# Optimization experiments

Measured on AMD Instinct MI355X. Metric: run time of the kernel, lower is better.

Reference implementation:

```python
import jax, jax.numpy as jnp
import numpy as np

B, T, E, H, S = 4, 4096, 1024, 16, 64
D = E // H  # head_dim = 64
ROPE_BASE = 10000.0


def _rotate_half(x):
    # interleaved rotate: out[..., 2i] = -x[..., 2i+1]; out[..., 2i+1] = x[..., 2i]
    x1 = x[..., ::2]
    x2 = x[..., 1::2]
    return jnp.stack([-x2, x1], axis=-1).reshape(x.shape)


def _rope_cos_sin(t, d):
    inv_freq = 1.0 / (ROPE_BASE ** (jnp.arange(0, d, 2, dtype=jnp.float32) / d))
    freqs = jnp.arange(t, dtype=jnp.float32)[:, None] * inv_freq[None, :]  # [t, d/2]
    emb = jnp.concatenate([freqs, freqs], axis=-1)  # [t, d]
    # broadcast over batch and heads for q/k of shape [b, t, h, d]
    return jnp.cos(emb)[None, :, None, :], jnp.sin(emb)[None, :, None, :]


def setup_inputs() -> dict:
    key = jax.random.key(0)
    ks = jax.random.split(key, 6)
    s = E ** -0.5
    return {
        "x": jax.random.normal(ks[0], (B, T, E), dtype=jnp.float32),
        "Wq": jax.random.normal(ks[1], (E, E), dtype=jnp.float32) * s,
        "Wk": jax.random.normal(ks[2], (E, E), dtype=jnp.float32) * s,
        "Wv": jax.random.normal(ks[3], (E, E), dtype=jnp.float32) * s,
        "Wout": jax.random.normal(ks[4], (E, E), dtype=jnp.float32) * s,
        "slot_keys": jax.random.normal(ks[5], (H, S, D), dtype=jnp.float32) * (D ** -0.5),
    }


def reference(x, Wq, Wk, Wv, Wout, slot_keys):
    b, t, e = x.shape
    h, s_slots, d = slot_keys.shape
    scale = d ** -0.5

    q = (x @ Wq.T).reshape(b, t, h, d)
    k = (x @ Wk.T).reshape(b, t, h, d)
    v = (x @ Wv.T).reshape(b, t, h, d)

    cos, sin = _rope_cos_sin(t, d)
    q = q * cos + _rotate_half(q) * sin
    k = k * cos + _rotate_half(k) * sin

    # write pass: route each token's value into memory slots
    write_logits = jnp.einsum('bthd,hsd->bths', k, slot_keys) * scale
    write_weights = jax.nn.softmax(write_logits, axis=-1)  # write_temperature = 1.0
    slot_state = jnp.einsum('bths,bthd->bshd', write_weights, v) / t

    # read pass: query the slot memory
    read_logits = jnp.einsum('bthd,bshd->bths', q, slot_state) * scale
    read_weights = jax.nn.softmax(read_logits, axis=-1)  # read_temperature = 1.0
    read_out = jnp.einsum('bths,bshd->bthd', read_weights, slot_state)

    return read_out.reshape(b, t, e) @ Wout.T
```

## Files before the change

### kernel.cpp

```cpp
#include <hip/hip_runtime.h>
#include <cstdint>
#include <cstddef>

#define BB 4
#define TT 4096
#define EE 1024
#define HH 16
#define SSLOTS 64
#define DD 64
#define MM (BB*TT)

typedef unsigned short u16;
typedef __attribute__((ext_vector_type(8))) short s16x8;
typedef __attribute__((ext_vector_type(4))) float f32x4;
typedef __attribute__((ext_vector_type(8))) unsigned short us8v;
typedef __attribute__((ext_vector_type(4))) unsigned short us4v;

#define MFMA16(a, b, c) __builtin_amdgcn_mfma_f32_16x16x32_bf16((a), (b), (c), 0, 0, 0)

__device__ __forceinline__ u16 f2bf(float x) {
  union { float f; uint32_t u; } c; c.f = x;
  uint32_t u = c.u;
  u += 0x7fffu + ((u >> 16) & 1u);
  return (u16)(u >> 16);
}

__device__ __forceinline__ float bf2f(u16 x) {
  union { uint32_t u; float f; } c; c.u = ((uint32_t)x) << 16;
  return c.f;
}

__device__ __forceinline__ void async16(const void* g, void* l) {
  auto lp = reinterpret_cast<__attribute__((address_space(3))) void*>(
      reinterpret_cast<uintptr_t>(l));
  auto gp = reinterpret_cast<const __attribute__((address_space(1))) void*>(
      reinterpret_cast<uintptr_t>(g));
  __builtin_amdgcn_global_load_lds(gp, lp, 16, 0, 0);
}

__device__ __forceinline__ us8v rope8(us8v kv, const float* __restrict__ rcp,
                                      const float* __restrict__ rsp) {
  float e[8];
#pragma unroll
  for (int m = 0; m < 8; ++m) e[m] = bf2f((u16)kv[m]);
  us8v o;
#pragma unroll
  for (int j = 0; j < 4; ++j) {
    float c0 = rcp[2 * j], c1 = rcp[2 * j + 1];
    float s0 = rsp[2 * j], s1 = rsp[2 * j + 1];
    o[2 * j]     = f2bf(e[2 * j] * c0 - e[2 * j + 1] * s0);
    o[2 * j + 1] = f2bf(e[2 * j + 1] * c1 + e[2 * j] * s1);
  }
  return o;
}

__global__ __launch_bounds__(256) void k_cvt(const float* __restrict__ s,
                                             u16* __restrict__ d, int n) {
  int i = (blockIdx.x * 256 + threadIdx.x) * 4;
  if (i >= n) return;
  float4 v = *(const float4*)(s + i);
  us4v o = { f2bf(v.x), f2bf(v.y), f2bf(v.z), f2bf(v.w) };
  *(us4v*)(d + i) = o;
}

__global__ __launch_bounds__(256) void k_rope(float* __restrict__ rc, float* __restrict__ rs) {
  int i = blockIdx.x * 256 + threadIdx.x;
  if (i >= TT * 32) return;
  int t = i >> 5, f = i & 31;
  double invf = pow(10000.0, -(double)(2 * f) / 64.0);
  double th = fmod((double)t * invf, 6.28318530717958647692528676655900577);
  rc[i] = (float)cos(th);
  rs[i] = (float)sin(th);
}

__device__ __forceinline__ void gemm_tile_128(const u16* __restrict__ Ablk,
                                              const u16* __restrict__ Bblk,
                                              int K, u16* As, u16* Bs,
                                              f32x4 acc[4][4]) {
  const int tid = threadIdx.x;
  const int lane = tid & 63, wave = tid >> 6;
  const int l16 = lane & 15, q8 = (lane >> 4) * 8;
  const int wm = (wave >> 1) * 64, wn = (wave & 1) * 64;
  const int ar = tid >> 2, ac = (tid & 3) * 8;
  const u16* Ag0 = Ablk + (size_t)ar * K + ac;
  const u16* Ag1 = Ablk + (size_t)(ar + 64) * K + ac;
  const u16* Bg0 = Bblk + (size_t)ar * K + ac;
  const u16* Bg1 = Bblk + (size_t)(ar + 64) * K + ac;
  u16* Al0 = As + ar * 32 + ac;
  u16* Al1 = As + (ar + 64) * 32 + ac;
  u16* Bl0 = Bs + ar * 32 + ac;
  u16* Bl1 = Bs + (ar + 64) * 32 + ac;

  for (int k0 = 0; k0 < K; k0 += 32) {
    async16(Ag0 + k0, Al0);
    async16(Ag1 + k0, Al1);
    async16(Bg0 + k0, Bl0);
    async16(Bg1 + k0, Bl1);
    __syncthreads();
    s16x8 af[4], bf[4];
#pragma unroll
    for (int i = 0; i < 4; ++i) {
      af[i] = *(const s16x8*)(As + (wm + i * 16 + l16) * 32 + q8);
      bf[i] = *(const s16x8*)(Bs + (wn + i * 16 + l16) * 32 + q8);
    }
#pragma unroll
    for (int im = 0; im < 4; ++im)
#pragma unroll
      for (int in = 0; in < 4; ++in)
        acc[im][in] = MFMA16(af[im], bf[in], acc[im][in]);
    __syncthreads();
  }
}

__global__ __launch_bounds__(256) void k_gemm_qkv(const u16* __restrict__ A,
                                                  const u16* __restrict__ Bw,
                                                  u16* __restrict__ q16,
                                                  u16* __restrict__ k16,
                                                  u16* __restrict__ v16) {
  __shared__ u16 As[128 * 32];
  __shared__ u16 Bs[128 * 32];
  f32x4 acc[4][4];
#pragma unroll
  for (int i = 0; i < 4; ++i)
#pragma unroll
    for (int j = 0; j < 4; ++j) acc[i][j] = (f32x4){0.f, 0.f, 0.f, 0.f};

  const int m0 = blockIdx.x * 128;
  const int n0g = blockIdx.y * 128;
  gemm_tile_128(A + (size_t)m0 * 1024, Bw + (size_t)n0g * 1024, 1024, As, Bs, acc);

  const int tid = threadIdx.x, lane = tid & 63, wave = tid >> 6;
  const int l16 = lane & 15, q4 = lane >> 4;
  const int wm = (wave >> 1) * 64, wn = (wave & 1) * 64;
  const int which = n0g >> 10;
  const int nb = n0g & 1023;
  u16* dst = (which == 0) ? q16 : ((which == 1) ? k16 : v16);

#pragma unroll
  for (int im = 0; im < 4; ++im)
#pragma unroll
    for (int in = 0; in < 4; ++in)
#pragma unroll
      for (int reg = 0; reg < 4; ++reg) {
        float v = acc[im][in][reg];
        int m = m0 + wm + im * 16 + q4 * 4 + reg;
        int nn = nb + wn + in * 16 + l16;
        int b = m >> 12, t = m & 4095;
        int h = nn >> 6, d = nn & 63;
        dst[((size_t)(b * HH + h) * TT + t) * 64 + d] = f2bf(v);
      }
}

__global__ __launch_bounds__(256) void k_gemm_out(const u16* __restrict__ A,
                                                  const u16* __restrict__ Bw,
                                                  float* __restrict__ C) {
  __shared__ u16 As[128 * 32];
  __shared__ u16 Bs[128 * 32];
  f32x4 acc[4][4];
#pragma unroll
  for (int i = 0; i < 4; ++i)
#pragma unroll
    for (int j = 0; j < 4; ++j) acc[i][j] = (f32x4){0.f, 0.f, 0.f, 0.f};

  const int m0 = blockIdx.x * 128;
  const int n0 = blockIdx.y * 128;
  gemm_tile_128(A + (size_t)m0 * 1024, Bw + (size_t)n0 * 1024, 1024, As, Bs, acc);

  const int tid = threadIdx.x, lane = tid & 63, wave = tid >> 6;
  const int l16 = lane & 15, q4 = lane >> 4;
  const int wm = (wave >> 1) * 64, wn = (wave & 1) * 64;
#pragma unroll
  for (int im = 0; im < 4; ++im)
#pragma unroll
    for (int in = 0; in < 4; ++in)
#pragma unroll
      for (int reg = 0; reg < 4; ++reg) {
        int m = m0 + wm + im * 16 + q4 * 4 + reg;
        int n = n0 + wn + in * 16 + l16;
        C[(size_t)m * 1024 + n] = acc[im][in][reg];
      }
}

__global__ __launch_bounds__(256) void k_stage2(const u16* __restrict__ K16g,
                                                const u16* __restrict__ V16g,
                                                const float* __restrict__ SKg,
                                                const float* __restrict__ rc,
                                                const float* __restrict__ rs,
                                                float* __restrict__ SSb) {
  const int tid = threadIdx.x, lane = tid & 63, wave = tid >> 6;
  const int l16 = lane & 15, q4 = lane >> 4, q8 = q4 * 8;
  const int bh = blockIdx.x >> 4, cb = blockIdx.x & 15;
  const int h = bh & 15;

  __shared__ u16 Ks[128 * 88];
  __shared__ u16 Vs[64 * 136];
  __shared__ u16 SKs[64 * 88];
  u16* ww = Ks;

  const float* skh = SKg + (size_t)h * (SSLOTS * DD);
  for (int i = tid; i < 4096; i += 256)
    SKs[(i >> 6) * 88 + (i & 63)] = f2bf(skh[i]);

  f32x4 a2[4];
#pragma unroll
  for (int in = 0; in < 4; ++in) a2[in] = (f32x4){0.f, 0.f, 0.f, 0.f};

  const int w32 = wave * 32;
  for (int cc = 0; cc < 2; ++cc) {
    const int tg0 = cb * 256 + cc * 128;
    __syncthreads();

    const u16* ks = K16g + ((size_t)bh * TT + tg0) * 64;
    for (int idx = tid; idx < 1024; idx += 256) {
      int t = idx >> 3, p = idx & 7;
      us8v kv = *(const us8v*)(ks + (size_t)t * 64 + p * 8);
      int fi = (tg0 + t) * 32 + ((p * 8) & 31);
      us8v kr = rope8(kv, rc + fi, rs + fi);
      *(us8v*)&Ks[t * 88 + p * 8] = kr;
    }
    const u16* vsrc = V16g + ((size_t)bh * TT + tg0) * 64;
    for (int idx = tid; idx < 1024; idx += 256) {
      int t = idx & 127, dg = idx >> 7;
      us8v vv = *(const us8v*)(vsrc + (size_t)t * 64 + dg * 8);
#pragma unroll
      for (int j = 0; j < 8; ++j) Vs[(dg * 8 + j) * 136 + t] = vv[j];
    }
    __syncthreads();

    f32x4 a1[2][4];
#pragma unroll
    for (int im = 0; im < 2; ++im)
#pragma unroll
      for (int in = 0; in < 4; ++in) a1[im][in] = (f32x4){0.f, 0.f, 0.f, 0.f};
#pragma unroll
    for (int ksx = 0; ksx < 2; ++ksx) {
      s16x8 afr0 = *(const s16x8*)&Ks[(w32 + l16) * 88 + ksx * 32 + q8];
      s16x8 afr1 = *(const s16x8*)&Ks[(w32 + 16 + l16) * 88 + ksx * 32 + q8];
#pragma unroll
      for (int in = 0; in < 4; ++in) {
        s16x8 bfr = *(const s16x8*)&SKs[(in * 16 + l16) * 88 + ksx * 32 + q8];
        a1[0][in] = MFMA16(afr0, bfr, a1[0][in]);
        a1[1][in] = MFMA16(afr1, bfr, a1[1][in]);
      }
    }
    __syncthreads();

#pragma unroll
    for (int im = 0; im < 2; ++im)
#pragma unroll
      for (int reg = 0; reg < 4; ++reg) {
        float v0 = a1[im][0][reg] * 0.125f, v1 = a1[im][1][reg] * 0.125f;
        float v2 = a1[im][2][reg] * 0.125f, v3 = a1[im][3][reg] * 0.125f;
        float mx = fmaxf(fmaxf(v0, v1), fmaxf(v2, v3));
#pragma unroll
        for (int m = 1; m < 16; m <<= 1) mx = fmaxf(mx, __shfl_xor(mx, m));
        float e0 = __expf(v0 - mx), e1 = __expf(v1 - mx);
        float e2 = __expf(v2 - mx), e3 = __expf(v3 - mx);
        float sm = e0 + e1 + e2 + e3;
#pragma unroll
        for (int m = 1; m < 16; m <<= 1) sm += __shfl_xor(sm, m);
        float inv = 1.0f / sm;
        int tl = w32 + im * 16 + q4 * 4 + reg;
        ww[(l16) * 136 + tl]      = f2bf(e0 * inv);
        ww[(16 + l16) * 136 + tl] = f2bf(e1 * inv);
        ww[(32 + l16) * 136 + tl] = f2bf(e2 * inv);
        ww[(48 + l16) * 136 + tl] = f2bf(e3 * inv);
      }
    __syncthreads();

#pragma unroll
    for (int ksx = 0; ksx < 4; ++ksx) {
      s16x8 afr = *(const s16x8*)&ww[(wave * 16 + l16) * 136 + ksx * 32 + q8];
#pragma unroll
      for (int in = 0; in < 4; ++in) {
        s16x8 bfr = *(const s16x8*)&Vs[(in * 16 + l16) * 136 + ksx * 32 + q8];
        a2[in] = MFMA16(afr, bfr, a2[in]);
      }
    }
  }

  const float invT = 1.0f / (float)TT;
#pragma unroll
  for (int in = 0; in < 4; ++in)
#pragma unroll
    for (int reg = 0; reg < 4; ++reg) {
      int s = wave * 16 + q4 * 4 + reg;
      int d = in * 16 + l16;
      atomicAdd(&SSb[(size_t)bh * 4096 + s * 64 + d], a2[in][reg] * invT);
    }
}

__global__ __launch_bounds__(256) void k_stage3(const u16* __restrict__ Q16g,
                                                const float* __restrict__ SSg,
                                                const float* __restrict__ rc,
                                                const float* __restrict__ rs,
                                                u16* __restrict__ RO) {
  const int tid = threadIdx.x, lane = tid & 63, wave = tid >> 6;
  const int l16 = lane & 15, q4 = lane >> 4, q8 = q4 * 8;
  const int bh = blockIdx.x >> 4, ck = blockIdx.x & 15;
  const int b = bh >> 4, h = bh & 15;
  const int tg0 = ck * 256;

  __shared__ u16 Qs[256 * 88];
  __shared__ u16 ss_sd[64 * 88];
  __shared__ u16 ss_ds[64 * 88];
  u16* RWs = Qs;

  const float* ssp = SSg + (size_t)bh * 4096;
  for (int i = tid; i < 4096; i += 256) {
    u16 u = f2bf(ssp[i]);
    int s = i >> 6, d = i & 63;
    ss_sd[s * 88 + d] = u;
    ss_ds[d * 88 + s] = u;
  }
  const u16* qsrc = Q16g + ((size_t)bh * TT + tg0) * 64;
  for (int idx = tid; idx < 2048; idx += 256) {
    int t = idx >> 3, p = idx & 7;
    us8v qv = *(const us8v*)(qsrc + (size_t)t * 64 + p * 8);
    int fi = (tg0 + t) * 32 + ((p * 8) & 31);
    us8v qr = rope8(qv, rc + fi, rs + fi);
    *(us8v*)&Qs[t * 88 + p * 8] = qr;
  }
  __syncthreads();

  const int w64 = wave * 64;
  f32x4 a3[4][4];
#pragma unroll
  for (int i = 0; i < 4; ++i)
#pragma unroll
    for (int j = 0; j < 4; ++j) a3[i][j] = (f32x4){0.f, 0.f, 0.f, 0.f};
#pragma unroll
  for (int ksx = 0; ksx < 2; ++ksx) {
    s16x8 afr[4];
#pragma unroll
    for (int im = 0; im < 4; ++im)
      afr[im] = *(const s16x8*)&Qs[(w64 + im * 16 + l16) * 88 + ksx * 32 + q8];
#pragma unroll
    for (int in = 0; in < 4; ++in) {
      s16x8 bfr = *(const s16x8*)&ss_sd[(in * 16 + l16) * 88 + ksx * 32 + q8];
#pragma unroll
      for (int im = 0; im < 4; ++im) a3[im][in] = MFMA16(afr[im], bfr, a3[im][in]);
    }
  }
  __syncthreads();

#pragma unroll
  for (int im = 0; im < 4; ++im)
#pragma unroll
    for (int reg = 0; reg < 4; ++reg) {
      float v0 = a3[im][0][reg] * 0.125f, v1 = a3[im][1][reg] * 0.125f;
      float v2 = a3[im][2][reg] * 0.125f, v3 = a3[im][3][reg] * 0.125f;
      float mx = fmaxf(fmaxf(v0, v1), fmaxf(v2, v3));
#pragma unroll
      for (int m = 1; m < 16; m <<= 1) mx = fmaxf(mx, __shfl_xor(mx, m));
      float e0 = __expf(v0 - mx), e1 = __expf(v1 - mx);
      float e2 = __expf(v2 - mx), e3 = __expf(v3 - mx);
      float sm = e0 + e1 + e2 + e3;
#pragma unroll
      for (int m = 1; m < 16; m <<= 1) sm += __shfl_xor(sm, m);
      float inv = 1.0f / sm;
      int tl = w64 + im * 16 + q4 * 4 + reg;
      RWs[tl * 88 + l16]      = f2bf(e0 * inv);
      RWs[tl * 88 + 16 + l16] = f2bf(e1 * inv);
      RWs[tl * 88 + 32 + l16] = f2bf(e2 * inv);
      RWs[tl * 88 + 48 + l16] = f2bf(e3 * inv);
    }
  __syncthreads();

  f32x4 a4[4][4];
#pragma unroll
  for (int i = 0; i < 4; ++i)
#pragma unroll
    for (int j = 0; j < 4; ++j) a4[i][j] = (f32x4){0.f, 0.f, 0.f, 0.f};
#pragma unroll
  for (int ksx = 0; ksx < 2; ++ksx) {
    s16x8 afr[4];
#pragma unroll
    for (int im = 0; im < 4; ++im)
      afr[im] = *(const s16x8*)&RWs[(w64 + im * 16 + l16) * 88 + ksx * 32 + q8];
#pragma unroll
    for (int in = 0; in < 4; ++in) {
      s16x8 bfr = *(const s16x8*)&ss_ds[(in * 16 + l16) * 88 + ksx * 32 + q8];
#pragma unroll
      for (int im = 0; im < 4; ++im) a4[im][in] = MFMA16(afr[im], bfr, a4[im][in]);
    }
  }

#pragma unroll
  for (int im = 0; im < 4; ++im)
#pragma unroll
    for (int in = 0; in < 4; ++in)
#pragma unroll
      for (int reg = 0; reg < 4; ++reg) {
        int t = tg0 + w64 + im * 16 + q4 * 4 + reg;
        int d = in * 16 + l16;
        RO[((size_t)b * TT + t) * 1024 + h * 64 + d] = f2bf(a4[im][in][reg]);
      }
}

extern "C" void kernel_launch(void* const* d_in, const int* in_sizes, int n_in,
                              void* d_out, int out_size, void* d_ws, size_t ws_size,
                              hipStream_t stream) {
  const float* x  = (const float*)d_in[0];
  const float* Wq = (const float*)d_in[1];
  const float* Wk = (const float*)d_in[2];
  const float* Wv = (const float*)d_in[3];
  const float* Wo = (const float*)d_in[4];
  const float* SK = (const float*)d_in[5];
  float* out = (float*)d_out;

  char* w = (char*)d_ws;
  u16* x16 = (u16*)w;   w += (size_t)MM * EE * 2;
  u16* W16 = (u16*)w;   w += (size_t)3 * EE * EE * 2;
  u16* Wo16 = (u16*)w;  w += (size_t)EE * EE * 2;
  u16* Q16 = (u16*)w;   w += (size_t)BB * HH * TT * DD * 2;
  u16* K16 = (u16*)w;   w += (size_t)BB * HH * TT * DD * 2;
  u16* V16 = (u16*)w;   w += (size_t)BB * HH * TT * DD * 2;
  float* SSb = (float*)w; w += (size_t)BB * HH * SSLOTS * DD * 4;
  float* rc = (float*)w;  w += (size_t)TT * 32 * 4;
  float* rs = (float*)w;  w += (size_t)TT * 32 * 4;
  u16* RO16 = x16;

  if ((size_t)(w - (char*)d_ws) > ws_size) return;

  k_cvt<<<16384, 256, 0, stream>>>(x, x16, MM * EE);
  k_cvt<<<1024, 256, 0, stream>>>(Wq, W16, EE * EE);
  k_cvt<<<1024, 256, 0, stream>>>(Wk, W16 + EE * EE, EE * EE);
  k_cvt<<<1024, 256, 0, stream>>>(Wv, W16 + 2 * EE * EE, EE * EE);
  k_cvt<<<1024, 256, 0, stream>>>(Wo, Wo16, EE * EE);
  k_rope<<<512, 256, 0, stream>>>(rc, rs);

  k_gemm_qkv<<<dim3(MM / 128, 3 * EE / 128), 256, 0, stream>>>(x16, W16, Q16, K16, V16);

  hipMemsetAsync(SSb, 0, (size_t)BB * HH * SSLOTS * DD * 4, stream);
  k_stage2<<<1024, 256, 0, stream>>>(K16, V16, SK, rc, rs, SSb);
  k_stage3<<<1024, 256, 0, stream>>>(Q16, SSb, rc, rs, RO16);

  k_gemm_out<<<dim3(MM / 128, EE / 128), 256, 0, stream>>>(RO16, Wo16, out);
}
```

Measured before the change: 381.9 us.

## Merge weight conversions, swap GEMM grid order, retile stage2 and stage3

Folds the four weight-conversion launches into one kernel that picks source and destination by block index. Swaps the GEMM grid axes so consecutive blocks share the same row tile of A, which should improve L2 reuse of activations. Stage2 now covers 512 tokens per block with half as many blocks, cutting atomic adds. Stage3 uses 128-token tiles with twice as many blocks, for smaller LDS use and more occupancy.

```diff
diff --git a/kernel.cpp b/kernel.cpp
--- a/kernel.cpp
+++ b/kernel.cpp
@@ -58,6 +58,21 @@
                                              u16* __restrict__ d, int n) {
   int i = (blockIdx.x * 256 + threadIdx.x) * 4;
   if (i >= n) return;
+  float4 v = *(const float4*)(s + i);
+  us4v o = { f2bf(v.x), f2bf(v.y), f2bf(v.z), f2bf(v.w) };
+  *(us4v*)(d + i) = o;
+}
+
+__global__ __launch_bounds__(256) void k_cvt4(const float* __restrict__ w0,
+                                              const float* __restrict__ w1,
+                                              const float* __restrict__ w2,
+                                              const float* __restrict__ w3,
+                                              u16* __restrict__ dW,
+                                              u16* __restrict__ dWo) {
+  int sel = blockIdx.x >> 10;
+  const float* s = (sel == 0) ? w0 : (sel == 1) ? w1 : (sel == 2) ? w2 : w3;
+  u16* d = (sel < 3) ? (dW + (size_t)sel * EE * EE) : dWo;
+  int i = ((blockIdx.x & 1023) * 256 + threadIdx.x) * 4;
   float4 v = *(const float4*)(s + i);
   us4v o = { f2bf(v.x), f2bf(v.y), f2bf(v.z), f2bf(v.w) };
   *(us4v*)(d + i) = o;
@@ -125,8 +140,8 @@
 #pragma unroll
     for (int j = 0; j < 4; ++j) acc[i][j] = (f32x4){0.f, 0.f, 0.f, 0.f};
 
-  const int m0 = blockIdx.x * 128;
-  const int n0g = blockIdx.y * 128;
+  const int m0 = blockIdx.y * 128;
+  const int n0g = blockIdx.x * 128;
   gemm_tile_128(A + (size_t)m0 * 1024, Bw + (size_t)n0g * 1024, 1024, As, Bs, acc);
 
   const int tid = threadIdx.x, lane = tid & 63, wave = tid >> 6;
@@ -162,8 +177,8 @@
 #pragma unroll
     for (int j = 0; j < 4; ++j) acc[i][j] = (f32x4){0.f, 0.f, 0.f, 0.f};
 
-  const int m0 = blockIdx.x * 128;
-  const int n0 = blockIdx.y * 128;
+  const int m0 = blockIdx.y * 128;
+  const int n0 = blockIdx.x * 128;
   gemm_tile_128(A + (size_t)m0 * 1024, Bw + (size_t)n0 * 1024, 1024, As, Bs, acc);
 
   const int tid = threadIdx.x, lane = tid & 63, wave = tid >> 6;
@@ -189,7 +204,7 @@
                                                 float* __restrict__ SSb) {
   const int tid = threadIdx.x, lane = tid & 63, wave = tid >> 6;
   const int l16 = lane & 15, q4 = lane >> 4, q8 = q4 * 8;
-  const int bh = blockIdx.x >> 4, cb = blockIdx.x & 15;
+  const int bh = blockIdx.x >> 3, cb = blockIdx.x & 7;
   const int h = bh & 15;
 
   __shared__ u16 Ks[128 * 88];
@@ -206,8 +221,8 @@
   for (int in = 0; in < 4; ++in) a2[in] = (f32x4){0.f, 0.f, 0.f, 0.f};
 
   const int w32 = wave * 32;
-  for (int cc = 0; cc < 2; ++cc) {
-    const int tg0 = cb * 256 + cc * 128;
+  for (int cc = 0; cc < 4; ++cc) {
+    const int tg0 = cb * 512 + cc * 128;
     __syncthreads();
 
     const u16* ks = K16g + ((size_t)bh * TT + tg0) * 64;
@@ -297,11 +312,11 @@
                                                 u16* __restrict__ RO) {
   const int tid = threadIdx.x, lane = tid & 63, wave = tid >> 6;
   const int l16 = lane & 15, q4 = lane >> 4, q8 = q4 * 8;
-  const int bh = blockIdx.x >> 4, ck = blockIdx.x & 15;
+  const int bh = blockIdx.x >> 5, ck = blockIdx.x & 31;
   const int b = bh >> 4, h = bh & 15;
-  const int tg0 = ck * 256;
-
-  __shared__ u16 Qs[256 * 88];
+  const int tg0 = ck * 128;
+
+  __shared__ u16 Qs[128 * 88];
   __shared__ u16 ss_sd[64 * 88];
   __shared__ u16 ss_ds[64 * 88];
   u16* RWs = Qs;
@@ -314,7 +329,7 @@
     ss_ds[d * 88 + s] = u;
   }
   const u16* qsrc = Q16g + ((size_t)bh * TT + tg0) * 64;
-  for (int idx = tid; idx < 2048; idx += 256) {
+  for (int idx = tid; idx < 1024; idx += 256) {
     int t = idx >> 3, p = idx & 7;
     us8v qv = *(const us8v*)(qsrc + (size_t)t * 64 + p * 8);
     int fi = (tg0 + t) * 32 + ((p * 8) & 31);
@@ -323,29 +338,29 @@
   }
   __syncthreads();
 
-  const int w64 = wave * 64;
-  f32x4 a3[4][4];
-#pragma unroll
-  for (int i = 0; i < 4; ++i)
+  const int w32 = wave * 32;
+  f32x4 a3[2][4];
+#pragma unroll
+  for (int i = 0; i < 2; ++i)
 #pragma unroll
     for (int j = 0; j < 4; ++j) a3[i][j] = (f32x4){0.f, 0.f, 0.f, 0.f};
 #pragma unroll
   for (int ksx = 0; ksx < 2; ++ksx) {
-    s16x8 afr[4];
-#pragma unroll
-    for (int im = 0; im < 4; ++im)
-      afr[im] = *(const s16x8*)&Qs[(w64 + im * 16 + l16) * 88 + ksx * 32 + q8];
+    s16x8 afr[2];
+#pragma unroll
+    for (int im = 0; im < 2; ++im)
+      afr[im] = *(const s16x8*)&Qs[(w32 + im * 16 + l16) * 88 + ksx * 32 + q8];
 #pragma unroll
     for (int in = 0; in < 4; ++in) {
       s16x8 bfr = *(const s16x8*)&ss_sd[(in * 16 + l16) * 88 + ksx * 32 + q8];
 #pragma unroll
-      for (int im = 0; im < 4; ++im) a3[im][in] = MFMA16(afr[im], bfr, a3[im][in]);
+      for (int im = 0; im < 2; ++im) a3[im][in] = MFMA16(afr[im], bfr, a3[im][in]);
     }
   }
   __syncthreads();
 
 #pragma unroll
-  for (int im = 0; im < 4; ++im)
+  for (int im = 0; im < 2; ++im)
 #pragma unroll
     for (int reg = 0; reg < 4; ++reg) {
       float v0 = a3[im][0][reg] * 0.125f, v1 = a3[im][1][reg] * 0.125f;
@@ -359,7 +374,7 @@
 #pragma unroll
       for (int m = 1; m < 16; m <<= 1) sm += __shfl_xor(sm, m);
       float inv = 1.0f / sm;
-      int tl = w64 + im * 16 + q4 * 4 + reg;
+      int tl = w32 + im * 16 + q4 * 4 + reg;
       RWs[tl * 88 + l16]      = f2bf(e0 * inv);
       RWs[tl * 88 + 16 + l16] = f2bf(e1 * inv);
       RWs[tl * 88 + 32 + l16] = f2bf(e2 * inv);
@@ -367,32 +382,32 @@
     }
   __syncthreads();
 
-  f32x4 a4[4][4];
-#pragma unroll
-  for (int i = 0; i < 4; ++i)
+  f32x4 a4[2][4];
+#pragma unroll
+  for (int i = 0; i < 2; ++i)
 #pragma unroll
     for (int j = 0; j < 4; ++j) a4[i][j] = (f32x4){0.f, 0.f, 0.f, 0.f};
 #pragma unroll
   for (int ksx = 0; ksx < 2; ++ksx) {
-    s16x8 afr[4];
-#pragma unroll
-    for (int im = 0; im < 4; ++im)
-      afr[im] = *(const s16x8*)&RWs[(w64 + im * 16 + l16) * 88 + ksx * 32 + q8];
+    s16x8 afr[2];
+#pragma unroll
+    for (int im = 0; im < 2; ++im)
+      afr[im] = *(const s16x8*)&RWs[(w32 + im * 16 + l16) * 88 + ksx * 32 + q8];
 #pragma unroll
     for (int in = 0; in < 4; ++in) {
       s16x8 bfr = *(const s16x8*)&ss_ds[(in * 16 + l16) * 88 + ksx * 32 + q8];
 #pragma unroll
-      for (int im = 0; im < 4; ++im) a4[im][in] = MFMA16(afr[im], bfr, a4[im][in]);
-    }
-  }
-
-#pragma unroll
-  for (int im = 0; im < 4; ++im)
+      for (int im = 0; im < 2; ++im) a4[im][in] = MFMA16(afr[im], bfr, a4[im][in]);
+    }
+  }
+
+#pragma unroll
+  for (int im = 0; im < 2; ++im)
 #pragma unroll
     for (int in = 0; in < 4; ++in)
 #pragma unroll
       for (int reg = 0; reg < 4; ++reg) {
-        int t = tg0 + w64 + im * 16 + q4 * 4 + reg;
+        int t = tg0 + w32 + im * 16 + q4 * 4 + reg;
         int d = in * 16 + l16;
         RO[((size_t)b * TT + t) * 1024 + h * 64 + d] = f2bf(a4[im][in][reg]);
       }
@@ -424,17 +439,14 @@
   if ((size_t)(w - (char*)d_ws) > ws_size) return;
 
   k_cvt<<<16384, 256, 0, stream>>>(x, x16, MM * EE);
-  k_cvt<<<1024, 256, 0, stream>>>(Wq, W16, EE * EE);
-  k_cvt<<<1024, 256, 0, stream>>>(Wk, W16 + EE * EE, EE * EE);
-  k_cvt<<<1024, 256, 0, stream>>>(Wv, W16 + 2 * EE * EE, EE * EE);
-  k_cvt<<<1024, 256, 0, stream>>>(Wo, Wo16, EE * EE);
+  k_cvt4<<<4096, 256, 0, stream>>>(Wq, Wk, Wv, Wo, W16, Wo16);
   k_rope<<<512, 256, 0, stream>>>(rc, rs);
 
-  k_gemm_qkv<<<dim3(MM / 128, 3 * EE / 128), 256, 0, stream>>>(x16, W16, Q16, K16, V16);
+  k_gemm_qkv<<<dim3(3 * EE / 128, MM / 128), 256, 0, stream>>>(x16, W16, Q16, K16, V16);
 
   hipMemsetAsync(SSb, 0, (size_t)BB * HH * SSLOTS * DD * 4, stream);
-  k_stage2<<<1024, 256, 0, stream>>>(K16, V16, SK, rc, rs, SSb);
-  k_stage3<<<1024, 256, 0, stream>>>(Q16, SSb, rc, rs, RO16);
-
-  k_gemm_out<<<dim3(MM / 128, EE / 128), 256, 0, stream>>>(RO16, Wo16, out);
-}
+  k_stage2<<<512, 256, 0, stream>>>(K16, V16, SK, rc, rs, SSb);
+  k_stage3<<<2048, 256, 0, stream>>>(Q16, SSb, rc, rs, RO16);
+
+  k_gemm_out<<<dim3(EE / 128, MM / 128), 256, 0, stream>>>(RO16, Wo16, out);
+}
```

After: 369.1 us. 3.3% less time.
